# Kernel tuning notes

Hardware: AMD Instinct MI355X
Metric: run time of the kernel (lower is better)

Reference implementation:

```python
import jax, jax.numpy as jnp
import numpy as np

K = 5          # receptive field
N_IN = 4       # inputs per LUT node
DEPTH = 2      # tree depth -> layer widths [16, 4, 1]


def lut_nodes(s, lut):
    """Differentiable DWN LUT nodes.
    s:   [P, C, N, n] selected inputs in [0,1]
    lut: [C, N, 2**n] raw LUT weights (sigmoid applied -> entries in (0,1))
    out[p,c,m] = sum_a sigmoid(lut[c,m,a]) * prod_j s_j^{bit_j(a)} (1-s_j)^{1-bit_j(a)}
    Evaluated by contracting one address bit at a time (bit j=0 most significant).
    """
    n = s.shape[-1]
    C, N = lut.shape[0], lut.shape[1]
    t = jax.nn.sigmoid(lut).reshape((C, N) + (2,) * n)  # [C,N,2,...,2]
    for j in reversed(range(n)):
        xb = s[..., j].reshape(s.shape[:-1] + (1,) * j)  # [P,C,N,1*j]
        t = t[..., 0] * (1.0 - xb) + t[..., 1] * xb
    return t  # [P, C, N]


def extract_patches(x):
    """nn.Unfold(kernel=K, stride=1, pad=0): x [B,Cin,H,W] -> [B*P, Cin*K*K]."""
    B, Cin, H, W = x.shape
    Hp, Wp = H - K + 1, W - K + 1
    cols = jnp.stack([x[:, :, i:i + Hp, j:j + Wp]
                      for i in range(K) for j in range(K)], axis=2)  # [B,Cin,K*K,Hp,Wp]
    patches = cols.reshape(B, Cin * K * K, Hp * Wp)
    return patches.transpose(0, 2, 1).reshape(B * Hp * Wp, Cin * K * K), (B, Hp, Wp)


def setup_inputs() -> dict:
    key = jax.random.key(0)
    ks = jax.random.split(key, 7)
    C = 64
    return {
        "x": jax.random.uniform(ks[0], (32, 1, 32, 32), dtype=jnp.float32),
        "lut0": jax.random.normal(ks[1], (C, 16, 16), dtype=jnp.float32),
        "lut1": jax.random.normal(ks[2], (C, 4, 16), dtype=jnp.float32),
        "lut2": jax.random.normal(ks[3], (C, 1, 16), dtype=jnp.float32),
        "idx0": jax.random.randint(ks[4], (C, 16, N_IN), 0, 25, dtype=jnp.int32),
        "idx1": jax.random.randint(ks[5], (C, 4, N_IN), 0, 16, dtype=jnp.int32),
        "idx2": jax.random.randint(ks[6], (C, 1, N_IN), 0, 4, dtype=jnp.int32),
    }


def reference(x, lut0, lut1, lut2, idx0, idx1, idx2):
    patches, (B, Hp, Wp) = extract_patches(x)          # [P, 25]
    C = lut0.shape[0]
    # layer 0: gather raw patch features per channel/node
    s0 = patches[:, idx0]                              # [P, C, 16, 4]
    h0 = lut_nodes(s0, lut0)                           # [P, C, 16]
    # layer 1: per-channel gather from previous layer
    s1 = jnp.take_along_axis(h0[:, :, None, :], idx1[None], axis=-1)  # [P, C, 4, 4]
    h1 = lut_nodes(s1, lut1)                           # [P, C, 4]
    # layer 2 (root)
    s2 = jnp.take_along_axis(h1[:, :, None, :], idx2[None], axis=-1)  # [P, C, 1, 4]
    h2 = lut_nodes(s2, lut2)[..., 0]                   # [P, C]
    out = h2.reshape(B, Hp * Wp, C).transpose(0, 2, 1).reshape(B, C, Hp, Wp)
    return out
```

## Files before the change

### kernel.cpp

```cpp
#include <hip/hip_runtime.h>
#include <math.h>

#define KK 5
#define WPOUT 28
#define PPI 784
#define NCH 64
#define NPATCH 25088
#define NPAIR 12544
#define THREADS 256
#define NNODE 21

typedef float f32x32 __attribute__((ext_vector_type(32)));
typedef float f32x16 __attribute__((ext_vector_type(16)));
typedef _Float16 h2  __attribute__((ext_vector_type(2)));

static __device__ __forceinline__ h2 u2h(unsigned u) { return __builtin_bit_cast(h2, u); }
static __device__ __forceinline__ unsigned h2u(h2 h) { return __builtin_bit_cast(unsigned, h); }
static __device__ __forceinline__ unsigned f2u(float f) { return __builtin_bit_cast(unsigned, f); }
static __device__ __forceinline__ float u2f(unsigned u) { return __builtin_bit_cast(float, u); }

static __device__ __forceinline__ unsigned packpair(float a, float b) {
    const auto pk = __builtin_amdgcn_cvt_pkrtz(a, b);
    return __builtin_bit_cast(unsigned, pk);
}

template <int ODD>
static __device__ __forceinline__ unsigned pkfma_splat(unsigned s, unsigned d, unsigned e) {
    unsigned r;
    if constexpr (ODD)
        asm("v_pk_fma_f16 %0, %1, %2, %3 op_sel:[0,1,1] op_sel_hi:[1,1,1]"
            : "=v"(r) : "v"(s), "v"(d), "v"(e));
    else
        asm("v_pk_fma_f16 %0, %1, %2, %3 op_sel:[0,0,0] op_sel_hi:[1,0,0]"
            : "=v"(r) : "v"(s), "v"(d), "v"(e));
    return r;
}

static __device__ __forceinline__ unsigned node_pair(uint4 E, uint4 D,
                                                     unsigned s0, unsigned s1,
                                                     unsigned s2, unsigned s3) {
    const unsigned Ea[4] = { E.x, E.y, E.z, E.w };
    const unsigned Da[4] = { D.x, D.y, D.z, D.w };
    unsigned v[8];
#pragma unroll
    for (int k = 0; k < 8; k += 2) {
        v[k]     = pkfma_splat<0>(s3, Da[k >> 1], Ea[k >> 1]);
        v[k + 1] = pkfma_splat<1>(s3, Da[k >> 1], Ea[k >> 1]);
    }
    const h2 s2h = u2h(s2), s1h = u2h(s1), s0h = u2h(s0);
    h2 w[4];
#pragma unroll
    for (int k = 0; k < 4; ++k) {
        const h2 ve = u2h(v[2 * k]), vo = u2h(v[2 * k + 1]);
        w[k] = s2h * (vo - ve) + ve;
    }
    const h2 u0 = s1h * (w[1] - w[0]) + w[0];
    const h2 u1 = s1h * (w[3] - w[2]) + w[2];
    return h2u(s0h * (u1 - u0) + u0);
}

__global__ __launch_bounds__(THREADS)
void dwn_conv_lut_kernel(const float* __restrict__ x,
                         const float* __restrict__ lut0,
                         const float* __restrict__ lut1,
                         const float* __restrict__ lut2,
                         const int*   __restrict__ idx0,
                         const int*   __restrict__ idx1,
                         const int*   __restrict__ idx2,
                         float*       __restrict__ out)
{
    __shared__ __align__(16) _Float16 lut[NNODE][16];

    const int tid = threadIdx.x;
    const int c   = blockIdx.y;

    if (tid < NNODE * 8) {
        const int k = tid & 7, node = tid >> 3;
        const float* src;
        if (node < 16)      src = lut0 + (c * 16 + node) * 16;
        else if (node < 20) src = lut1 + (c * 4 + (node - 16)) * 16;
        else                src = lut2 + c * 16;
        const float a = src[2 * k], b = src[2 * k + 1];
        const float ea = 1.0f / (1.0f + __expf(-a));
        const float eb = 1.0f / (1.0f + __expf(-b));
        lut[node][k]     = (_Float16)ea;
        lut[node][k + 8] = (_Float16)(eb - ea);
    }

    const int pi = blockIdx.x * THREADS + tid;
    const int p  = 2 * pi;
    const int b  = p / PPI;
    const int q  = p - b * PPI;
    const int i  = q / WPOUT;
    const int j  = q - i * WPOUT;

    const float* rp0 = x + b * 1024 + i * 32 + j;
    f32x32 pv;
#pragma unroll
    for (int di = 0; di < KK; ++di) {
        const float2* r2 = (const float2*)(rp0 + di * 32);
        const float2 w01 = r2[0], w23 = r2[1], w45 = r2[2];
        const float w[6] = { w01.x, w01.y, w23.x, w23.y, w45.x, w45.y };
#pragma unroll
        for (int dj = 0; dj < KK; ++dj) {
            pv[di * 5 + dj] = u2f(packpair(w[dj], w[dj + 1]));
        }
    }

    __syncthreads();

    const int* id0 = idx0 + c * 64;
    f32x16 h0;
#pragma unroll
    for (int m = 0; m < 16; ++m) {
        const uint4* row = (const uint4*)&lut[m][0];
        const uint4 E = row[0], D = row[1];
        const int i0 = __builtin_amdgcn_readfirstlane(id0[m * 4 + 0]);
        const int i1 = __builtin_amdgcn_readfirstlane(id0[m * 4 + 1]);
        const int i2 = __builtin_amdgcn_readfirstlane(id0[m * 4 + 2]);
        const int i3 = __builtin_amdgcn_readfirstlane(id0[m * 4 + 3]);
        const unsigned r = node_pair(E, D, f2u(pv[i0]), f2u(pv[i1]), f2u(pv[i2]), f2u(pv[i3]));
        h0[m] = u2f(r);
    }

    const int* id1 = idx1 + c * 16;
    unsigned h1[4];
#pragma unroll
    for (int m = 0; m < 4; ++m) {
        const uint4* row = (const uint4*)&lut[16 + m][0];
        const uint4 E = row[0], D = row[1];
        const int i0 = __builtin_amdgcn_readfirstlane(id1[m * 4 + 0]);
        const int i1 = __builtin_amdgcn_readfirstlane(id1[m * 4 + 1]);
        const int i2 = __builtin_amdgcn_readfirstlane(id1[m * 4 + 2]);
        const int i3 = __builtin_amdgcn_readfirstlane(id1[m * 4 + 3]);
        h1[m] = node_pair(E, D, f2u(h0[i0]), f2u(h0[i1]), f2u(h0[i2]), f2u(h0[i3]));
    }

    const int* id2 = idx2 + c * 4;
    unsigned s[4];
#pragma unroll
    for (int jj = 0; jj < 4; ++jj) {
        const int ii = __builtin_amdgcn_readfirstlane(id2[jj]);
        s[jj] = (ii == 0) ? h1[0] : (ii == 1) ? h1[1] : (ii == 2) ? h1[2] : h1[3];
    }
    const uint4* row2 = (const uint4*)&lut[20][0];
    const h2 r = u2h(node_pair(row2[0], row2[1], s[0], s[1], s[2], s[3]));

    float2* o = (float2*)(out + (b * NCH + c) * PPI + q);
    *o = make_float2((float)r[0], (float)r[1]);
}

extern "C" void kernel_launch(void* const* d_in, const int* in_sizes, int n_in,
                              void* d_out, int out_size, void* d_ws, size_t ws_size,
                              hipStream_t stream) {
    const float* x    = (const float*)d_in[0];
    const float* lut0 = (const float*)d_in[1];
    const float* lut1 = (const float*)d_in[2];
    const float* lut2 = (const float*)d_in[3];
    const int*   idx0 = (const int*)d_in[4];
    const int*   idx1 = (const int*)d_in[5];
    const int*   idx2 = (const int*)d_in[6];
    float* out = (float*)d_out;

    dim3 grid(NPAIR / THREADS, NCH);
    dim3 block(THREADS);
    dwn_conv_lut_kernel<<<grid, block, 0, stream>>>(x, lut0, lut1, lut2,
                                                    idx0, idx1, idx2, out);
}
```

Baseline: 22.47 us.

## Precompute sigmoid LUTs in prep kernel and read them as scalar operands

Moves the per-block sigmoid and fp16 packing of LUT weights into a separate small prep kernel that writes interleaved (value, delta) pairs to workspace. The main kernel drops its shared-memory staging and __syncthreads, and loads the wave-uniform LUT rows directly so they can live in scalar registers, used as SGPR operands of v_pk_fma_f16. This removes redundant per-block sigmoid work and LDS traffic, at the cost of an extra kernel launch and a dependency between the two kernels.

```diff
diff --git a/kernel.cpp b/kernel.cpp
--- a/kernel.cpp
+++ b/kernel.cpp
@@ -5,7 +5,6 @@
 #define WPOUT 28
 #define PPI 784
 #define NCH 64
-#define NPATCH 25088
 #define NPAIR 12544
 #define THREADS 256
 #define NNODE 21
@@ -13,6 +12,7 @@
 typedef float f32x32 __attribute__((ext_vector_type(32)));
 typedef float f32x16 __attribute__((ext_vector_type(16)));
 typedef _Float16 h2  __attribute__((ext_vector_type(2)));
+typedef unsigned u32x8 __attribute__((ext_vector_type(8)));
 
 static __device__ __forceinline__ h2 u2h(unsigned u) { return __builtin_bit_cast(h2, u); }
 static __device__ __forceinline__ unsigned h2u(h2 h) { return __builtin_bit_cast(unsigned, h); }
@@ -24,29 +24,19 @@
     return __builtin_bit_cast(unsigned, pk);
 }
 
-template <int ODD>
-static __device__ __forceinline__ unsigned pkfma_splat(unsigned s, unsigned d, unsigned e) {
+static __device__ __forceinline__ unsigned pkfma_ed(unsigned s, unsigned X) {
     unsigned r;
-    if constexpr (ODD)
-        asm("v_pk_fma_f16 %0, %1, %2, %3 op_sel:[0,1,1] op_sel_hi:[1,1,1]"
-            : "=v"(r) : "v"(s), "v"(d), "v"(e));
-    else
-        asm("v_pk_fma_f16 %0, %1, %2, %3 op_sel:[0,0,0] op_sel_hi:[1,0,0]"
-            : "=v"(r) : "v"(s), "v"(d), "v"(e));
+    asm("v_pk_fma_f16 %0, %1, %2, %2 op_sel:[0,1,0] op_sel_hi:[1,1,0]"
+        : "=v"(r) : "v"(s), "s"(X));
     return r;
 }
 
-static __device__ __forceinline__ unsigned node_pair(uint4 E, uint4 D,
-                                                     unsigned s0, unsigned s1,
-                                                     unsigned s2, unsigned s3) {
-    const unsigned Ea[4] = { E.x, E.y, E.z, E.w };
-    const unsigned Da[4] = { D.x, D.y, D.z, D.w };
+static __device__ __forceinline__ unsigned node_pair_s(const u32x8 ED,
+                                                       unsigned s0, unsigned s1,
+                                                       unsigned s2, unsigned s3) {
     unsigned v[8];
 #pragma unroll
-    for (int k = 0; k < 8; k += 2) {
-        v[k]     = pkfma_splat<0>(s3, Da[k >> 1], Ea[k >> 1]);
-        v[k + 1] = pkfma_splat<1>(s3, Da[k >> 1], Ea[k >> 1]);
-    }
+    for (int k = 0; k < 8; ++k) v[k] = pkfma_ed(s3, ED[k]);
     const h2 s2h = u2h(s2), s1h = u2h(s1), s0h = u2h(s0);
     h2 w[4];
 #pragma unroll
@@ -59,33 +49,40 @@
     return h2u(s0h * (u1 - u0) + u0);
 }
 
+__global__ void sigmoid_prep(const float* __restrict__ lut0,
+                             const float* __restrict__ lut1,
+                             const float* __restrict__ lut2,
+                             unsigned* __restrict__ ws)
+{
+    const int t = blockIdx.x * 256 + threadIdx.x;
+    if (t >= NCH * NNODE * 8) return;
+    const int k    = t & 7;
+    const int node = (t >> 3) % NNODE;
+    const int c    = t / (8 * NNODE);
+    const float* src;
+    if (node < 16)      src = lut0 + (c * 16 + node) * 16;
+    else if (node < 20) src = lut1 + (c * 4 + (node - 16)) * 16;
+    else                src = lut2 + c * 16;
+    const float a = src[2 * k], b = src[2 * k + 1];
+    const float ea = 1.0f / (1.0f + __expf(-a));
+    const float eb = 1.0f / (1.0f + __expf(-b));
+    const _Float16 e = (_Float16)ea;
+    const _Float16 d = (_Float16)(eb - ea);
+    ws[(c * NNODE + node) * 8 + k] =
+        (unsigned)__builtin_bit_cast(unsigned short, e) |
+        ((unsigned)__builtin_bit_cast(unsigned short, d) << 16);
+}
+
 __global__ __launch_bounds__(THREADS)
 void dwn_conv_lut_kernel(const float* __restrict__ x,
-                         const float* __restrict__ lut0,
-                         const float* __restrict__ lut1,
-                         const float* __restrict__ lut2,
+                         const unsigned* __restrict__ ws,
                          const int*   __restrict__ idx0,
                          const int*   __restrict__ idx1,
                          const int*   __restrict__ idx2,
                          float*       __restrict__ out)
 {
-    __shared__ __align__(16) _Float16 lut[NNODE][16];
-
     const int tid = threadIdx.x;
     const int c   = blockIdx.y;
-
-    if (tid < NNODE * 8) {
-        const int k = tid & 7, node = tid >> 3;
-        const float* src;
-        if (node < 16)      src = lut0 + (c * 16 + node) * 16;
-        else if (node < 20) src = lut1 + (c * 4 + (node - 16)) * 16;
-        else                src = lut2 + c * 16;
-        const float a = src[2 * k], b = src[2 * k + 1];
-        const float ea = 1.0f / (1.0f + __expf(-a));
-        const float eb = 1.0f / (1.0f + __expf(-b));
-        lut[node][k]     = (_Float16)ea;
-        lut[node][k + 8] = (_Float16)(eb - ea);
-    }
 
     const int pi = blockIdx.x * THREADS + tid;
     const int p  = 2 * pi;
@@ -107,33 +104,30 @@
         }
     }
 
-    __syncthreads();
+    const unsigned* lutc = ws + c * (NNODE * 8);
+    const int* id0 = idx0 + c * 64;
 
-    const int* id0 = idx0 + c * 64;
     f32x16 h0;
 #pragma unroll
     for (int m = 0; m < 16; ++m) {
-        const uint4* row = (const uint4*)&lut[m][0];
-        const uint4 E = row[0], D = row[1];
+        const u32x8 ED = *(const u32x8*)(lutc + m * 8);
         const int i0 = __builtin_amdgcn_readfirstlane(id0[m * 4 + 0]);
         const int i1 = __builtin_amdgcn_readfirstlane(id0[m * 4 + 1]);
         const int i2 = __builtin_amdgcn_readfirstlane(id0[m * 4 + 2]);
         const int i3 = __builtin_amdgcn_readfirstlane(id0[m * 4 + 3]);
-        const unsigned r = node_pair(E, D, f2u(pv[i0]), f2u(pv[i1]), f2u(pv[i2]), f2u(pv[i3]));
-        h0[m] = u2f(r);
+        h0[m] = u2f(node_pair_s(ED, f2u(pv[i0]), f2u(pv[i1]), f2u(pv[i2]), f2u(pv[i3])));
     }
 
     const int* id1 = idx1 + c * 16;
     unsigned h1[4];
 #pragma unroll
     for (int m = 0; m < 4; ++m) {
-        const uint4* row = (const uint4*)&lut[16 + m][0];
-        const uint4 E = row[0], D = row[1];
+        const u32x8 ED = *(const u32x8*)(lutc + (16 + m) * 8);
         const int i0 = __builtin_amdgcn_readfirstlane(id1[m * 4 + 0]);
         const int i1 = __builtin_amdgcn_readfirstlane(id1[m * 4 + 1]);
         const int i2 = __builtin_amdgcn_readfirstlane(id1[m * 4 + 2]);
         const int i3 = __builtin_amdgcn_readfirstlane(id1[m * 4 + 3]);
-        h1[m] = node_pair(E, D, f2u(h0[i0]), f2u(h0[i1]), f2u(h0[i2]), f2u(h0[i3]));
+        h1[m] = node_pair_s(ED, f2u(h0[i0]), f2u(h0[i1]), f2u(h0[i2]), f2u(h0[i3]));
     }
 
     const int* id2 = idx2 + c * 4;
@@ -143,8 +137,8 @@
         const int ii = __builtin_amdgcn_readfirstlane(id2[jj]);
         s[jj] = (ii == 0) ? h1[0] : (ii == 1) ? h1[1] : (ii == 2) ? h1[2] : h1[3];
     }
-    const uint4* row2 = (const uint4*)&lut[20][0];
-    const h2 r = u2h(node_pair(row2[0], row2[1], s[0], s[1], s[2], s[3]));
+    const u32x8 ED2 = *(const u32x8*)(lutc + 20 * 8);
+    const h2 r = u2h(node_pair_s(ED2, s[0], s[1], s[2], s[3]));
 
     float2* o = (float2*)(out + (b * NCH + c) * PPI + q);
     *o = make_float2((float)r[0], (float)r[1]);
@@ -161,9 +155,14 @@
     const int*   idx1 = (const int*)d_in[5];
     const int*   idx2 = (const int*)d_in[6];
     float* out = (float*)d_out;
+    unsigned* ws = (unsigned*)d_ws;
 
-    dim3 grid(NPAIR / THREADS, NCH);
-    dim3 block(THREADS);
-    dwn_conv_lut_kernel<<<grid, block, 0, stream>>>(x, lut0, lut1, lut2,
-                                                    idx0, idx1, idx2, out);
+    {
+        const int total = NCH * NNODE * 8;
+        sigmoid_prep<<<dim3((total + 255) / 256), dim3(256), 0, stream>>>(lut0, lut1, lut2, ws);
+    }
+    {
+        dim3 grid(NPAIR / THREADS, NCH);
+        dwn_conv_lut_kernel<<<grid, dim3(THREADS), 0, stream>>>(x, ws, idx0, idx1, idx2, out);
+    }
 }
```

Result: slower. 27.46 us (+22.2%).
